# Optimization experiments

Hardware: AMD Instinct MI355X
Metric: run time of the kernel (lower is better)

The kernel has to match this reference:

```python
import jax, jax.numpy as jnp
import numpy as np
from jax import lax

N_NODES = 150_000
N_EDGES = 1_500_000
N_GRAPHS = 150          # batch_size(30) * sequence_length(5), hardcoded in forward
BATCH_SIZE = 30
SEQ_LEN = 5
IN_F = 1
HID = 100               # gcn_hidden_size == lstm_hidden_size


def setup_inputs() -> dict:
    key = jax.random.key(0)
    ks = jax.random.split(key, 12)
    x = jax.random.normal(ks[0], (N_NODES, IN_F), dtype=jnp.float32)
    edge_index = jax.random.randint(ks[1], (2, N_EDGES), 0, N_NODES, dtype=jnp.int32)
    # 150 graphs of 1000 nodes each (contiguous, as PyG batching produces)
    batch = jnp.repeat(jnp.arange(N_GRAPHS, dtype=jnp.int32), N_NODES // N_GRAPHS)
    s = 0.1
    params = {
        # GCNConv layer 1: Linear(no bias) weight stored [in, out]; separate bias
        "W1": jax.random.normal(ks[2], (IN_F, HID), jnp.float32) * s,
        "b1": jnp.zeros((HID,), jnp.float32),
        # GCNConv layer 2
        "W2": jax.random.normal(ks[3], (HID, HID), jnp.float32) * s,
        "b2": jnp.zeros((HID,), jnp.float32),
        # LSTM (PyTorch gate order i,f,g,o), weights [4H, in]/[4H, H]
        "W_ih": jax.random.normal(ks[4], (4 * HID, HID), jnp.float32) * s,
        "W_hh": jax.random.normal(ks[5], (4 * HID, HID), jnp.float32) * s,
        "b_ih": jnp.zeros((4 * HID,), jnp.float32),
        "b_hh": jnp.zeros((4 * HID,), jnp.float32),
        # output head Linear(HID, 1)
        "W_out": jax.random.normal(ks[6], (1, HID), jnp.float32) * s,
        "b_out": jnp.zeros((1,), jnp.float32),
    }
    return {"x": x, "edge_index": edge_index, "batch": batch, **params}


def _gcn_conv(x, src, dst, W, b, n_nodes):
    """PyG GCNConv: h = W x; out = D^-1/2 (A+I) D^-1/2 h + b."""
    h = x @ W  # [N, HID]
    deg = jax.ops.segment_sum(jnp.ones_like(dst, dtype=h.dtype), dst, num_segments=n_nodes)
    dinv = lax.rsqrt(deg)  # deg >= 1 thanks to self loops
    norm = dinv[src] * dinv[dst]  # [E+N]
    msg = h[src] * norm[:, None]  # gather + scale (memory-bound hot loop)
    out = jax.ops.segment_sum(msg, dst, num_segments=n_nodes)
    return out + b


def _lstm_last_hidden(xs, W_ih, W_hh, b_ih, b_hh):
    """xs: [B, T, H] -> last hidden state [B, H] (single-layer LSTM)."""
    B = xs.shape[0]
    H = W_hh.shape[1]
    h0 = jnp.zeros((B, H), xs.dtype)
    c0 = jnp.zeros((B, H), xs.dtype)

    def step(carry, xt):
        h, c = carry
        gates = xt @ W_ih.T + h @ W_hh.T + (b_ih + b_hh)
        i, f, g, o = jnp.split(gates, 4, axis=-1)
        c = jax.nn.sigmoid(f) * c + jax.nn.sigmoid(i) * jnp.tanh(g)
        h = jax.nn.sigmoid(o) * jnp.tanh(c)
        return (h, c), None

    (h_last, _), _ = lax.scan(step, (h0, c0), jnp.swapaxes(xs, 0, 1))
    return h_last


def reference(x, edge_index, batch, W1, b1, W2, b2, W_ih, W_hh, b_ih, b_hh, W_out, b_out):
    n_nodes = x.shape[0]
    loops = jnp.arange(n_nodes, dtype=edge_index.dtype)
    src = jnp.concatenate([edge_index[0], loops])
    dst = jnp.concatenate([edge_index[1], loops])

    h = _gcn_conv(x, src, dst, W1, b1, n_nodes)
    h = _gcn_conv(h, src, dst, W2, b2, n_nodes)

    # global mean pool over 150 graphs
    sums = jax.ops.segment_sum(h, batch, num_segments=N_GRAPHS)
    cnts = jax.ops.segment_sum(jnp.ones((n_nodes,), h.dtype), batch, num_segments=N_GRAPHS)
    pooled = sums / jnp.maximum(cnts, 1.0)[:, None]  # [150, HID]

    seq = pooled.reshape(BATCH_SIZE, SEQ_LEN, -1)  # [30, 5, HID]
    h_last = _lstm_last_hidden(seq, W_ih, W_hh, b_ih, b_hh)
    prediction = h_last @ W_out.T + b_out  # [30, 1]
    return prediction
```

## Files before the change

### kernel.cpp

```cpp
#include <hip/hip_runtime.h>
#include <math.h>

#define N_NODES   150000
#define N_EDGES   1500000
#define N_GRAPHS  150
#define HID       100
#define BATCH     30
#define SEQ       5
#define NODES_PER_GRAPH 1000

#define NPB       256
#define NB        ((N_NODES + NPB - 1) / NPB)
#define SBLK      512
#define EPB       2932

__global__ __launch_bounds__(256) void k_s1(const int* __restrict__ dst,
                                            int* __restrict__ blockBase) {
    __shared__ int hist[NB];
    int t = threadIdx.x;
    for (int i = t; i < NB; i += 256) hist[i] = 0;
    __syncthreads();
    int base = blockIdx.x * EPB;
    int end  = min(base + EPB, N_EDGES);
    for (int i = base + t * 4; i < end; i += 1024) {
        int4 d = *reinterpret_cast<const int4*>(dst + i);
        atomicAdd(&hist[d.x >> 8], 1);
        atomicAdd(&hist[d.y >> 8], 1);
        atomicAdd(&hist[d.z >> 8], 1);
        atomicAdd(&hist[d.w >> 8], 1);
    }
    __syncthreads();
    for (int j = t; j < NB; j += 256)
        blockBase[blockIdx.x * NB + j] = hist[j];
}

__global__ __launch_bounds__(512) void k_colscan(int* __restrict__ blockBase,
                                                 int* __restrict__ bucketCount) {
    __shared__ int v[SBLK];
    int j = blockIdx.x;
    int t = threadIdx.x;
    int val = blockBase[t * NB + j];
    v[t] = val;
    __syncthreads();
    for (int off = 1; off < SBLK; off <<= 1) {
        int w = (t >= off) ? v[t - off] : 0;
        __syncthreads();
        v[t] += w;
        __syncthreads();
    }
    blockBase[t * NB + j] = v[t] - val;
    if (t == SBLK - 1) bucketCount[j] = v[t];
}

__global__ __launch_bounds__(256) void k_scan(const int* __restrict__ cnt,
                                              int* __restrict__ start) {
    __shared__ int part[256];
    int t = threadIdx.x;
    int j0 = t * 3;
    int s = 0;
    #pragma unroll
    for (int k = 0; k < 3; ++k) { int j = j0 + k; if (j < NB) s += cnt[j]; }
    part[t] = s;
    __syncthreads();
    for (int off = 1; off < 256; off <<= 1) {
        int w = (t >= off) ? part[t - off] : 0;
        __syncthreads();
        part[t] += w;
        __syncthreads();
    }
    int run = part[t] - s;
    #pragma unroll
    for (int k = 0; k < 3; ++k) {
        int j = j0 + k;
        if (j < NB) { start[j] = run; run += cnt[j]; }
    }
    if (t == 0) start[NB] = N_EDGES;
}

__global__ __launch_bounds__(256) void k_s2(const int* __restrict__ src,
                                            const int* __restrict__ dst,
                                            const int* __restrict__ bucketStart,
                                            const int* __restrict__ blockBase,
                                            unsigned int* __restrict__ sorted) {
    __shared__ int cursor[NB];
    __shared__ int baseS[NB];
    int t = threadIdx.x;
    const int* bb = blockBase + blockIdx.x * NB;
    for (int i = t; i < NB; i += 256) {
        cursor[i] = 0;
        baseS[i] = bucketStart[i] + bb[i];
    }
    __syncthreads();
    int base = blockIdx.x * EPB;
    int end  = min(base + EPB, N_EDGES);
    for (int i = base + t * 4; i < end; i += 1024) {
        int4 s4 = *reinterpret_cast<const int4*>(src + i);
        int4 d4 = *reinterpret_cast<const int4*>(dst + i);
        int bs[4] = { d4.x >> 8, d4.y >> 8, d4.z >> 8, d4.w >> 8 };
        int sv[4] = { s4.x, s4.y, s4.z, s4.w };
        int dl[4] = { d4.x & 255, d4.y & 255, d4.z & 255, d4.w & 255 };
        #pragma unroll
        for (int k = 0; k < 4; ++k) {
            int b = bs[k];
            int idx = atomicAdd(&cursor[b], 1);
            sorted[baseS[b] + idx] = ((unsigned int)sv[k] << 8) | (unsigned int)dl[k];
        }
    }
}

__global__ __launch_bounds__(256) void k_accA(const unsigned int* __restrict__ sorted,
                                              const int* __restrict__ bucketStart,
                                              const float* __restrict__ x,
                                              float2* __restrict__ p) {
    __shared__ int degI[2][NPB];
    int b = blockIdx.x;
    int t = threadIdx.x;
    int n0 = b << 8;
    int nn = min(NPB, N_NODES - n0);
    degI[0][t] = 0; degI[1][t] = 0;
    __syncthreads();
    int e0 = bucketStart[b], e1 = bucketStart[b + 1];
    int rep = t & 1;
    int e0a = min((e0 + 3) & ~3, e1);
    if (e0 + t < e0a) atomicAdd(&degI[rep][sorted[e0 + t] & 255], 1);
    int nvec = (e1 - e0a) >> 2;
    for (int v = t; v < nvec; v += 256) {
        uint4 u4 = *reinterpret_cast<const uint4*>(sorted + e0a + v * 4);
        atomicAdd(&degI[rep][u4.x & 255], 1);
        atomicAdd(&degI[rep][u4.y & 255], 1);
        atomicAdd(&degI[rep][u4.z & 255], 1);
        atomicAdd(&degI[rep][u4.w & 255], 1);
    }
    int tail0 = e0a + (nvec << 2);
    if (tail0 + t < e1) atomicAdd(&degI[rep][sorted[tail0 + t] & 255], 1);
    __syncthreads();
    if (t < nn) {
        float dv = 1.0f / sqrtf((float)(1 + degI[0][t] + degI[1][t]));
        p[n0 + t] = make_float2(dv, dv * x[n0 + t]);
    }
}

__global__ __launch_bounds__(256) void k_accB(const unsigned int* __restrict__ sorted,
                                              const int* __restrict__ bucketStart,
                                              const float2* __restrict__ p,
                                              float* __restrict__ agg1,
                                              float* __restrict__ wsum,
                                              float* __restrict__ a1s) {
    __shared__ float t1[2][NPB], t2[2][NPB];
    int b = blockIdx.x;
    int t = threadIdx.x;
    int n0 = b << 8;
    int nn = min(NPB, N_NODES - n0);
    t1[0][t] = 0.0f; t1[1][t] = 0.0f; t2[0][t] = 0.0f; t2[1][t] = 0.0f;
    __syncthreads();
    int e0 = bucketStart[b], e1 = bucketStart[b + 1];
    int rep = t & 1;
    int e0a = min((e0 + 3) & ~3, e1);
    if (e0 + t < e0a) {
        unsigned int u = sorted[e0 + t];
        float2 pv = p[u >> 8];
        atomicAdd(&t2[rep][u & 255], pv.x);
        atomicAdd(&t1[rep][u & 255], pv.y);
    }
    int nvec = (e1 - e0a) >> 2;
    for (int v = t; v < nvec; v += 256) {
        uint4 u4 = *reinterpret_cast<const uint4*>(sorted + e0a + v * 4);
        float2 p0 = p[u4.x >> 8];
        float2 p1 = p[u4.y >> 8];
        float2 p2 = p[u4.z >> 8];
        float2 p3 = p[u4.w >> 8];
        atomicAdd(&t2[rep][u4.x & 255], p0.x);
        atomicAdd(&t1[rep][u4.x & 255], p0.y);
        atomicAdd(&t2[rep][u4.y & 255], p1.x);
        atomicAdd(&t1[rep][u4.y & 255], p1.y);
        atomicAdd(&t2[rep][u4.z & 255], p2.x);
        atomicAdd(&t1[rep][u4.z & 255], p2.y);
        atomicAdd(&t2[rep][u4.w & 255], p3.x);
        atomicAdd(&t1[rep][u4.w & 255], p3.y);
    }
    int tail0 = e0a + (nvec << 2);
    if (tail0 + t < e1) {
        unsigned int u = sorted[tail0 + t];
        float2 pv = p[u >> 8];
        atomicAdd(&t2[rep][u & 255], pv.x);
        atomicAdd(&t1[rep][u & 255], pv.y);
    }
    __syncthreads();
    if (t < nn) {
        float2 pv = p[n0 + t];
        float dv = pv.x;
        float T1 = t1[0][t] + t1[1][t];
        float T2 = t2[0][t] + t2[1][t];
        float a = dv * T1 + dv * pv.y;
        agg1[n0 + t] = a;
        wsum[n0 + t] = dv * (T2 + dv);
        a1s[n0 + t]  = dv * a;
    }
}

__global__ __launch_bounds__(256) void k_accC(const unsigned int* __restrict__ sorted,
                                              const int* __restrict__ bucketStart,
                                              const float2* __restrict__ p,
                                              const float* __restrict__ agg1,
                                              const float* __restrict__ a1s,
                                              float* __restrict__ agg2) {
    __shared__ float ua[2][NPB];
    int b = blockIdx.x;
    int t = threadIdx.x;
    int n0 = b << 8;
    int nn = min(NPB, N_NODES - n0);
    ua[0][t] = 0.0f; ua[1][t] = 0.0f;
    __syncthreads();
    int e0 = bucketStart[b], e1 = bucketStart[b + 1];
    int rep = t & 1;
    int e0a = min((e0 + 3) & ~3, e1);
    if (e0 + t < e0a) {
        unsigned int u = sorted[e0 + t];
        atomicAdd(&ua[rep][u & 255], a1s[u >> 8]);
    }
    int nvec = (e1 - e0a) >> 2;
    for (int v = t; v < nvec; v += 256) {
        uint4 u4 = *reinterpret_cast<const uint4*>(sorted + e0a + v * 4);
        atomicAdd(&ua[rep][u4.x & 255], a1s[u4.x >> 8]);
        atomicAdd(&ua[rep][u4.y & 255], a1s[u4.y >> 8]);
        atomicAdd(&ua[rep][u4.z & 255], a1s[u4.z >> 8]);
        atomicAdd(&ua[rep][u4.w & 255], a1s[u4.w >> 8]);
    }
    int tail0 = e0a + (nvec << 2);
    if (tail0 + t < e1) {
        unsigned int u = sorted[tail0 + t];
        atomicAdd(&ua[rep][u & 255], a1s[u >> 8]);
    }
    __syncthreads();
    if (t < nn) {
        float dv = p[n0 + t].x;
        agg2[n0 + t] = dv * (ua[0][t] + ua[1][t] + dv * agg1[n0 + t]);
    }
}

__global__ __launch_bounds__(512) void k_pre(const float* __restrict__ agg2,
                                             const float* __restrict__ wsum,
                                             const float* __restrict__ W1,
                                             const float* __restrict__ b1,
                                             const float* __restrict__ W2,
                                             const float* __restrict__ b2,
                                             const float* __restrict__ W_ih,
                                             const float* __restrict__ b_ih,
                                             const float* __restrict__ b_hh,
                                             float* __restrict__ Xg) {
    int g = blockIdx.x;
    int t = threadIdx.x;
    __shared__ float xs[HID];
    __shared__ float red_a[512], red_w[512];

    const float* pa = agg2 + (size_t)g * NODES_PER_GRAPH;
    const float* pw = wsum + (size_t)g * NODES_PER_GRAPH;
    float sa = 0.0f, sw = 0.0f;
    for (int n = t; n < NODES_PER_GRAPH; n += 512) { sa += pa[n]; sw += pw[n]; }
    red_a[t] = sa; red_w[t] = sw;
    __syncthreads();
    for (int s = 256; s > 0; s >>= 1) {
        if (t < s) { red_a[t] += red_a[t + s]; red_w[t] += red_w[t + s]; }
        __syncthreads();
    }
    float mean_a = red_a[0] * (1.0f / NODES_PER_GRAPH);
    float mean_w = red_w[0] * (1.0f / NODES_PER_GRAPH);

    if (t < HID) {
        float a = 0.0f, c = 0.0f;
        for (int k = 0; k < HID; ++k) {
            float w2 = W2[k * HID + t];
            a += W1[k] * w2;
            c += b1[k] * w2;
        }
        xs[t] = mean_a * a + mean_w * c + b2[t];
    }
    __syncthreads();

    if (t < 4 * HID) {
        float acc = b_ih[t] + b_hh[t];
        const float4* wp = reinterpret_cast<const float4*>(W_ih + t * HID);
        #pragma unroll
        for (int q = 0; q < HID / 4; ++q) {
            float4 w4 = wp[q];
            acc += xs[4*q+0] * w4.x + xs[4*q+1] * w4.y + xs[4*q+2] * w4.z + xs[4*q+3] * w4.w;
        }
        Xg[(size_t)g * 4 * HID + t] = acc;
    }
}

__global__ __launch_bounds__(512) void k_rec(const float* __restrict__ Xg,
                                             const float* __restrict__ W_hh,
                                             const float* __restrict__ W_out,
                                             const float* __restrict__ b_out,
                                             float* __restrict__ outp) {
    int b = blockIdx.x;
    int t = threadIdx.x;
    __shared__ float hs[HID], cs[HID];
    __shared__ float gsb[4 * HID];
    __shared__ float red[512];

    float wreg[HID];
    if (t < 4 * HID) {
        const float4* wp = reinterpret_cast<const float4*>(W_hh + t * HID);
        #pragma unroll
        for (int q = 0; q < HID / 4; ++q) {
            float4 w4 = wp[q];
            wreg[4*q+0] = w4.x; wreg[4*q+1] = w4.y; wreg[4*q+2] = w4.z; wreg[4*q+3] = w4.w;
        }
    }
    if (t < HID) { hs[t] = 0.0f; cs[t] = 0.0f; }
    __syncthreads();

    for (int step = 0; step < SEQ; ++step) {
        if (t < 4 * HID) {
            float acc = Xg[(size_t)(b * SEQ + step) * 4 * HID + t];
            #pragma unroll
            for (int k = 0; k < HID; ++k)
                acc += hs[k] * wreg[k];
            gsb[t] = acc;
        }
        __syncthreads();
        if (t < HID) {
            float ig = 1.0f / (1.0f + expf(-gsb[t]));
            float fg = 1.0f / (1.0f + expf(-gsb[HID + t]));
            float gg = tanhf(gsb[2 * HID + t]);
            float og = 1.0f / (1.0f + expf(-gsb[3 * HID + t]));
            float c  = fg * cs[t] + ig * gg;
            cs[t] = c;
            hs[t] = og * tanhf(c);
        }
        __syncthreads();
    }

    float v = (t < HID) ? hs[t] * W_out[t] : 0.0f;
    red[t] = v;
    __syncthreads();
    for (int s = 256; s > 0; s >>= 1) {
        if (t < s) red[t] += red[t + s];
        __syncthreads();
    }
    if (t == 0) outp[b] = red[0] + b_out[0];
}

static inline char* align_up(char* p, size_t a) {
    return (char*)(((uintptr_t)p + (a - 1)) & ~(uintptr_t)(a - 1));
}

extern "C" void kernel_launch(void* const* d_in, const int* in_sizes, int n_in,
                              void* d_out, int out_size, void* d_ws, size_t ws_size,
                              hipStream_t stream) {
    const float* x    = (const float*)d_in[0];
    const int*   ei   = (const int*)d_in[1];
    const int*   srcp = ei;
    const int*   dstp = ei + N_EDGES;
    const float* W1   = (const float*)d_in[3];
    const float* b1   = (const float*)d_in[4];
    const float* W2   = (const float*)d_in[5];
    const float* b2   = (const float*)d_in[6];
    const float* W_ih = (const float*)d_in[7];
    const float* W_hh = (const float*)d_in[8];
    const float* b_ih = (const float*)d_in[9];
    const float* b_hh = (const float*)d_in[10];
    const float* W_out= (const float*)d_in[11];
    const float* b_out= (const float*)d_in[12];
    float* out = (float*)d_out;

    char* w = (char*)d_ws;
    int*  bucketCount = (int*)w;            w = align_up(w + NB * sizeof(int), 64);
    int*  bucketStart = (int*)w;            w = align_up(w + (NB + 1) * sizeof(int), 64);
    int*  blockBase   = (int*)w;            w = align_up(w + (size_t)SBLK * NB * sizeof(int), 64);
    unsigned int* sorted = (unsigned int*)w; w = align_up(w + (size_t)N_EDGES * sizeof(unsigned int), 64);
    float2* p   = (float2*)w;               w = align_up(w + (size_t)N_NODES * sizeof(float2), 64);
    float* agg1 = (float*)w;                w = align_up(w + (size_t)N_NODES * sizeof(float), 64);
    float* wsum = (float*)w;                w = align_up(w + (size_t)N_NODES * sizeof(float), 64);
    float* a1s  = (float*)w;                w = align_up(w + (size_t)N_NODES * sizeof(float), 64);
    float* agg2 = (float*)w;                w = align_up(w + (size_t)N_NODES * sizeof(float), 64);
    float* Xg   = (float*)w;                w = align_up(w + (size_t)N_GRAPHS * 4 * HID * sizeof(float), 64);

    k_s1     <<<SBLK, 256, 0, stream>>>(dstp, blockBase);
    k_colscan<<<NB, SBLK, 0, stream>>>(blockBase, bucketCount);
    k_scan   <<<1, 256, 0, stream>>>(bucketCount, bucketStart);
    k_s2     <<<SBLK, 256, 0, stream>>>(srcp, dstp, bucketStart, blockBase, sorted);
    k_accA   <<<NB, 256, 0, stream>>>(sorted, bucketStart, x, p);
    k_accB   <<<NB, 256, 0, stream>>>(sorted, bucketStart, p, agg1, wsum, a1s);
    k_accC   <<<NB, 256, 0, stream>>>(sorted, bucketStart, p, agg1, a1s, agg2);
    k_pre    <<<N_GRAPHS, 512, 0, stream>>>(agg2, wsum, W1, b1, W2, b2, W_ih, b_ih, b_hh, Xg);
    k_rec    <<<BATCH, 512, 0, stream>>>(Xg, W_hh, W_out, b_out, out);
}
```

Before: 95.90 us.

## Fold mean-pool into per-graph atomic sums and fuse pre-LSTM into recurrence kernel

Rewrites the second aggregation so it never materializes per-node agg2 or wsum. Each block reduces its edge contributions straight into per-graph sums with atomics, using the fact that pooling is linear. The graph-level gate projection is merged into the LSTM kernel, removing one launch and the Xg round trip. The float2 gather of (dv, dv*x) becomes a single float gather in the first aggregation, at the cost of extra block reductions and global float atomics whose summation order is nondeterministic.

```diff
diff --git a/kernel.cpp b/kernel.cpp
--- a/kernel.cpp
+++ b/kernel.cpp
@@ -53,9 +53,12 @@
 }
 
 __global__ __launch_bounds__(256) void k_scan(const int* __restrict__ cnt,
-                                              int* __restrict__ start) {
+                                              int* __restrict__ start,
+                                              float* __restrict__ graphA,
+                                              float* __restrict__ graphW) {
     __shared__ int part[256];
     int t = threadIdx.x;
+    if (t < N_GRAPHS) { graphA[t] = 0.0f; graphW[t] = 0.0f; }
     int j0 = t * 3;
     int s = 0;
     #pragma unroll
@@ -108,11 +111,34 @@
     }
 }
 
+__device__ __forceinline__ void graph_reduce_add(float val, int thresh, int nn,
+                                                 int g0, float* red, int t,
+                                                 float* __restrict__ gdst) {
+    red[t] = (t < thresh) ? val : 0.0f;
+    __syncthreads();
+    for (int s = 128; s > 0; s >>= 1) {
+        if (t < s) red[t] += red[t + s];
+        __syncthreads();
+    }
+    if (t == 0) atomicAdd(&gdst[g0], red[0]);
+    __syncthreads();
+    red[t] = (t >= thresh) ? val : 0.0f;
+    __syncthreads();
+    for (int s = 128; s > 0; s >>= 1) {
+        if (t < s) red[t] += red[t + s];
+        __syncthreads();
+    }
+    if (t == 0 && thresh < nn) atomicAdd(&gdst[g0 + 1], red[0]);
+}
+
 __global__ __launch_bounds__(256) void k_accA(const unsigned int* __restrict__ sorted,
                                               const int* __restrict__ bucketStart,
                                               const float* __restrict__ x,
-                                              float2* __restrict__ p) {
+                                              float* __restrict__ pd,
+                                              float* __restrict__ px,
+                                              float* __restrict__ graphW) {
     __shared__ int degI[2][NPB];
+    __shared__ float red[256];
     int b = blockIdx.x;
     int t = threadIdx.x;
     int n0 = b << 8;
@@ -134,137 +160,144 @@
     int tail0 = e0a + (nvec << 2);
     if (tail0 + t < e1) atomicAdd(&degI[rep][sorted[tail0 + t] & 255], 1);
     __syncthreads();
+    float val = 0.0f;
     if (t < nn) {
         float dv = 1.0f / sqrtf((float)(1 + degI[0][t] + degI[1][t]));
-        p[n0 + t] = make_float2(dv, dv * x[n0 + t]);
-    }
+        pd[n0 + t] = dv;
+        px[n0 + t] = dv * x[n0 + t];
+        val = dv * dv;
+    }
+    int g0 = n0 / 1000;
+    int thresh = (g0 + 1) * 1000 - n0;
+    graph_reduce_add(val, thresh, nn, g0, red, t, graphW);
 }
 
 __global__ __launch_bounds__(256) void k_accB(const unsigned int* __restrict__ sorted,
                                               const int* __restrict__ bucketStart,
-                                              const float2* __restrict__ p,
-                                              float* __restrict__ agg1,
-                                              float* __restrict__ wsum,
-                                              float* __restrict__ a1s) {
-    __shared__ float t1[2][NPB], t2[2][NPB];
+                                              const float* __restrict__ pd,
+                                              const float* __restrict__ px,
+                                              float2* __restrict__ pa2,
+                                              float* __restrict__ graphA) {
+    __shared__ float t1[2][NPB];
+    __shared__ float red[256];
     int b = blockIdx.x;
     int t = threadIdx.x;
     int n0 = b << 8;
     int nn = min(NPB, N_NODES - n0);
-    t1[0][t] = 0.0f; t1[1][t] = 0.0f; t2[0][t] = 0.0f; t2[1][t] = 0.0f;
+    t1[0][t] = 0.0f; t1[1][t] = 0.0f;
     __syncthreads();
     int e0 = bucketStart[b], e1 = bucketStart[b + 1];
     int rep = t & 1;
     int e0a = min((e0 + 3) & ~3, e1);
     if (e0 + t < e0a) {
         unsigned int u = sorted[e0 + t];
-        float2 pv = p[u >> 8];
-        atomicAdd(&t2[rep][u & 255], pv.x);
-        atomicAdd(&t1[rep][u & 255], pv.y);
+        atomicAdd(&t1[rep][u & 255], px[u >> 8]);
     }
     int nvec = (e1 - e0a) >> 2;
     for (int v = t; v < nvec; v += 256) {
         uint4 u4 = *reinterpret_cast<const uint4*>(sorted + e0a + v * 4);
-        float2 p0 = p[u4.x >> 8];
-        float2 p1 = p[u4.y >> 8];
-        float2 p2 = p[u4.z >> 8];
-        float2 p3 = p[u4.w >> 8];
-        atomicAdd(&t2[rep][u4.x & 255], p0.x);
-        atomicAdd(&t1[rep][u4.x & 255], p0.y);
-        atomicAdd(&t2[rep][u4.y & 255], p1.x);
-        atomicAdd(&t1[rep][u4.y & 255], p1.y);
-        atomicAdd(&t2[rep][u4.z & 255], p2.x);
-        atomicAdd(&t1[rep][u4.z & 255], p2.y);
-        atomicAdd(&t2[rep][u4.w & 255], p3.x);
-        atomicAdd(&t1[rep][u4.w & 255], p3.y);
+        float p0 = px[u4.x >> 8];
+        float p1 = px[u4.y >> 8];
+        float p2 = px[u4.z >> 8];
+        float p3 = px[u4.w >> 8];
+        atomicAdd(&t1[rep][u4.x & 255], p0);
+        atomicAdd(&t1[rep][u4.y & 255], p1);
+        atomicAdd(&t1[rep][u4.z & 255], p2);
+        atomicAdd(&t1[rep][u4.w & 255], p3);
     }
     int tail0 = e0a + (nvec << 2);
     if (tail0 + t < e1) {
         unsigned int u = sorted[tail0 + t];
-        float2 pv = p[u >> 8];
-        atomicAdd(&t2[rep][u & 255], pv.x);
-        atomicAdd(&t1[rep][u & 255], pv.y);
-    }
-    __syncthreads();
+        atomicAdd(&t1[rep][u & 255], px[u >> 8]);
+    }
+    __syncthreads();
+    float val = 0.0f;
     if (t < nn) {
-        float2 pv = p[n0 + t];
-        float dv = pv.x;
+        float dv = pd[n0 + t];
         float T1 = t1[0][t] + t1[1][t];
-        float T2 = t2[0][t] + t2[1][t];
-        float a = dv * T1 + dv * pv.y;
-        agg1[n0 + t] = a;
-        wsum[n0 + t] = dv * (T2 + dv);
-        a1s[n0 + t]  = dv * a;
-    }
-}
-
-__global__ __launch_bounds__(256) void k_accC(const unsigned int* __restrict__ sorted,
+        float agg1 = dv * T1 + dv * px[n0 + t];
+        float a1 = dv * agg1;
+        pa2[n0 + t] = make_float2(dv, a1);
+        val = dv * a1;
+    }
+    int g0 = n0 / 1000;
+    int thresh = (g0 + 1) * 1000 - n0;
+    graph_reduce_add(val, thresh, nn, g0, red, t, graphA);
+}
+
+__global__ __launch_bounds__(256) void k_accG(const unsigned int* __restrict__ sorted,
                                               const int* __restrict__ bucketStart,
-                                              const float2* __restrict__ p,
-                                              const float* __restrict__ agg1,
-                                              const float* __restrict__ a1s,
-                                              float* __restrict__ agg2) {
-    __shared__ float ua[2][NPB];
+                                              const float* __restrict__ pd,
+                                              const float2* __restrict__ pa2,
+                                              float* __restrict__ graphA,
+                                              float* __restrict__ graphW) {
+    __shared__ float dvl[NPB];
+    __shared__ float4 red4[256];
     int b = blockIdx.x;
     int t = threadIdx.x;
     int n0 = b << 8;
     int nn = min(NPB, N_NODES - n0);
-    ua[0][t] = 0.0f; ua[1][t] = 0.0f;
-    __syncthreads();
+    dvl[t] = (t < nn) ? pd[n0 + t] : 0.0f;
+    __syncthreads();
+    int g0 = n0 / 1000;
+    int thresh = (g0 + 1) * 1000 - n0;
+    float sa0 = 0.f, sa1 = 0.f, sw0 = 0.f, sw1 = 0.f;
     int e0 = bucketStart[b], e1 = bucketStart[b + 1];
-    int rep = t & 1;
     int e0a = min((e0 + 3) & ~3, e1);
-    if (e0 + t < e0a) {
-        unsigned int u = sorted[e0 + t];
-        atomicAdd(&ua[rep][u & 255], a1s[u >> 8]);
-    }
+    auto proc = [&](unsigned int u) {
+        int dl = (int)(u & 255);
+        float dvd = dvl[dl];
+        float2 v = pa2[u >> 8];
+        if (dl < thresh) { sw0 += dvd * v.x; sa0 += dvd * v.y; }
+        else             { sw1 += dvd * v.x; sa1 += dvd * v.y; }
+    };
+    if (e0 + t < e0a) proc(sorted[e0 + t]);
     int nvec = (e1 - e0a) >> 2;
     for (int v = t; v < nvec; v += 256) {
         uint4 u4 = *reinterpret_cast<const uint4*>(sorted + e0a + v * 4);
-        atomicAdd(&ua[rep][u4.x & 255], a1s[u4.x >> 8]);
-        atomicAdd(&ua[rep][u4.y & 255], a1s[u4.y >> 8]);
-        atomicAdd(&ua[rep][u4.z & 255], a1s[u4.z >> 8]);
-        atomicAdd(&ua[rep][u4.w & 255], a1s[u4.w >> 8]);
+        proc(u4.x); proc(u4.y); proc(u4.z); proc(u4.w);
     }
     int tail0 = e0a + (nvec << 2);
-    if (tail0 + t < e1) {
-        unsigned int u = sorted[tail0 + t];
-        atomicAdd(&ua[rep][u & 255], a1s[u >> 8]);
-    }
-    __syncthreads();
-    if (t < nn) {
-        float dv = p[n0 + t].x;
-        agg2[n0 + t] = dv * (ua[0][t] + ua[1][t] + dv * agg1[n0 + t]);
-    }
-}
-
-__global__ __launch_bounds__(512) void k_pre(const float* __restrict__ agg2,
-                                             const float* __restrict__ wsum,
-                                             const float* __restrict__ W1,
-                                             const float* __restrict__ b1,
-                                             const float* __restrict__ W2,
-                                             const float* __restrict__ b2,
-                                             const float* __restrict__ W_ih,
-                                             const float* __restrict__ b_ih,
-                                             const float* __restrict__ b_hh,
-                                             float* __restrict__ Xg) {
-    int g = blockIdx.x;
-    int t = threadIdx.x;
-    __shared__ float xs[HID];
-    __shared__ float red_a[512], red_w[512];
-
-    const float* pa = agg2 + (size_t)g * NODES_PER_GRAPH;
-    const float* pw = wsum + (size_t)g * NODES_PER_GRAPH;
-    float sa = 0.0f, sw = 0.0f;
-    for (int n = t; n < NODES_PER_GRAPH; n += 512) { sa += pa[n]; sw += pw[n]; }
-    red_a[t] = sa; red_w[t] = sw;
-    __syncthreads();
-    for (int s = 256; s > 0; s >>= 1) {
-        if (t < s) { red_a[t] += red_a[t + s]; red_w[t] += red_w[t + s]; }
-        __syncthreads();
-    }
-    float mean_a = red_a[0] * (1.0f / NODES_PER_GRAPH);
-    float mean_w = red_w[0] * (1.0f / NODES_PER_GRAPH);
+    if (tail0 + t < e1) proc(sorted[tail0 + t]);
+    red4[t] = make_float4(sa0, sa1, sw0, sw1);
+    __syncthreads();
+    for (int s = 128; s > 0; s >>= 1) {
+        if (t < s) {
+            red4[t].x += red4[t + s].x; red4[t].y += red4[t + s].y;
+            red4[t].z += red4[t + s].z; red4[t].w += red4[t + s].w;
+        }
+        __syncthreads();
+    }
+    if (t == 0) {
+        atomicAdd(&graphA[g0], red4[0].x);
+        atomicAdd(&graphW[g0], red4[0].z);
+        if (thresh < nn) {
+            atomicAdd(&graphA[g0 + 1], red4[0].y);
+            atomicAdd(&graphW[g0 + 1], red4[0].w);
+        }
+    }
+}
+
+__global__ __launch_bounds__(512) void k_tail(const float* __restrict__ graphA,
+                                              const float* __restrict__ graphW,
+                                              const float* __restrict__ W1,
+                                              const float* __restrict__ b1,
+                                              const float* __restrict__ W2,
+                                              const float* __restrict__ b2,
+                                              const float* __restrict__ W_ih,
+                                              const float* __restrict__ W_hh,
+                                              const float* __restrict__ b_ih,
+                                              const float* __restrict__ b_hh,
+                                              const float* __restrict__ W_out,
+                                              const float* __restrict__ b_out,
+                                              float* __restrict__ outp) {
+    int b = blockIdx.x;
+    int t = threadIdx.x;
+    __shared__ float v1[HID], v2[HID];
+    __shared__ float xs_l[SEQ][HID];
+    __shared__ float Xg_l[SEQ][4 * HID];
+    __shared__ float hs[HID], cs[HID], gsb[4 * HID];
+    __shared__ float red[512];
 
     if (t < HID) {
         float a = 0.0f, c = 0.0f;
@@ -273,36 +306,36 @@
             a += W1[k] * w2;
             c += b1[k] * w2;
         }
-        xs[t] = mean_a * a + mean_w * c + b2[t];
-    }
-    __syncthreads();
-
+        v1[t] = a; v2[t] = c;
+    }
+    __syncthreads();
+
+    if (t < SEQ * HID) {
+        int s = t / HID, j = t - s * HID;
+        int g = b * SEQ + s;
+        float ma = graphA[g] * (1.0f / NODES_PER_GRAPH);
+        float mw = graphW[g] * (1.0f / NODES_PER_GRAPH);
+        xs_l[s][j] = ma * v1[j] + mw * v2[j] + b2[j];
+    }
+    __syncthreads();
+
+    float wreg[HID];
     if (t < 4 * HID) {
-        float acc = b_ih[t] + b_hh[t];
         const float4* wp = reinterpret_cast<const float4*>(W_ih + t * HID);
         #pragma unroll
         for (int q = 0; q < HID / 4; ++q) {
             float4 w4 = wp[q];
-            acc += xs[4*q+0] * w4.x + xs[4*q+1] * w4.y + xs[4*q+2] * w4.z + xs[4*q+3] * w4.w;
-        }
-        Xg[(size_t)g * 4 * HID + t] = acc;
-    }
-}
-
-__global__ __launch_bounds__(512) void k_rec(const float* __restrict__ Xg,
-                                             const float* __restrict__ W_hh,
-                                             const float* __restrict__ W_out,
-                                             const float* __restrict__ b_out,
-                                             float* __restrict__ outp) {
-    int b = blockIdx.x;
-    int t = threadIdx.x;
-    __shared__ float hs[HID], cs[HID];
-    __shared__ float gsb[4 * HID];
-    __shared__ float red[512];
-
-    float wreg[HID];
-    if (t < 4 * HID) {
-        const float4* wp = reinterpret_cast<const float4*>(W_hh + t * HID);
+            wreg[4*q+0] = w4.x; wreg[4*q+1] = w4.y; wreg[4*q+2] = w4.z; wreg[4*q+3] = w4.w;
+        }
+        float bias = b_ih[t] + b_hh[t];
+        for (int s = 0; s < SEQ; ++s) {
+            float acc = bias;
+            #pragma unroll
+            for (int k = 0; k < HID; ++k)
+                acc += xs_l[s][k] * wreg[k];
+            Xg_l[s][t] = acc;
+        }
+        wp = reinterpret_cast<const float4*>(W_hh + t * HID);
         #pragma unroll
         for (int q = 0; q < HID / 4; ++q) {
             float4 w4 = wp[q];
@@ -314,7 +347,7 @@
 
     for (int step = 0; step < SEQ; ++step) {
         if (t < 4 * HID) {
-            float acc = Xg[(size_t)(b * SEQ + step) * 4 * HID + t];
+            float acc = Xg_l[step][t];
             #pragma unroll
             for (int k = 0; k < HID; ++k)
                 acc += hs[k] * wreg[k];
@@ -367,24 +400,23 @@
     float* out = (float*)d_out;
 
     char* w = (char*)d_ws;
-    int*  bucketCount = (int*)w;            w = align_up(w + NB * sizeof(int), 64);
-    int*  bucketStart = (int*)w;            w = align_up(w + (NB + 1) * sizeof(int), 64);
-    int*  blockBase   = (int*)w;            w = align_up(w + (size_t)SBLK * NB * sizeof(int), 64);
+    int*  bucketCount = (int*)w;             w = align_up(w + NB * sizeof(int), 64);
+    int*  bucketStart = (int*)w;             w = align_up(w + (NB + 1) * sizeof(int), 64);
+    int*  blockBase   = (int*)w;             w = align_up(w + (size_t)SBLK * NB * sizeof(int), 64);
     unsigned int* sorted = (unsigned int*)w; w = align_up(w + (size_t)N_EDGES * sizeof(unsigned int), 64);
-    float2* p   = (float2*)w;               w = align_up(w + (size_t)N_NODES * sizeof(float2), 64);
-    float* agg1 = (float*)w;                w = align_up(w + (size_t)N_NODES * sizeof(float), 64);
-    float* wsum = (float*)w;                w = align_up(w + (size_t)N_NODES * sizeof(float), 64);
-    float* a1s  = (float*)w;                w = align_up(w + (size_t)N_NODES * sizeof(float), 64);
-    float* agg2 = (float*)w;                w = align_up(w + (size_t)N_NODES * sizeof(float), 64);
-    float* Xg   = (float*)w;                w = align_up(w + (size_t)N_GRAPHS * 4 * HID * sizeof(float), 64);
+    float*  pd   = (float*)w;                w = align_up(w + (size_t)N_NODES * sizeof(float), 64);
+    float*  px   = (float*)w;                w = align_up(w + (size_t)N_NODES * sizeof(float), 64);
+    float2* pa2  = (float2*)w;               w = align_up(w + (size_t)N_NODES * sizeof(float2), 64);
+    float* graphA = (float*)w;               w = align_up(w + N_GRAPHS * sizeof(float), 64);
+    float* graphW = (float*)w;               w = align_up(w + N_GRAPHS * sizeof(float), 64);
 
     k_s1     <<<SBLK, 256, 0, stream>>>(dstp, blockBase);
     k_colscan<<<NB, SBLK, 0, stream>>>(blockBase, bucketCount);
-    k_scan   <<<1, 256, 0, stream>>>(bucketCount, bucketStart);
+    k_scan   <<<1, 256, 0, stream>>>(bucketCount, bucketStart, graphA, graphW);
     k_s2     <<<SBLK, 256, 0, stream>>>(srcp, dstp, bucketStart, blockBase, sorted);
-    k_accA   <<<NB, 256, 0, stream>>>(sorted, bucketStart, x, p);
-    k_accB   <<<NB, 256, 0, stream>>>(sorted, bucketStart, p, agg1, wsum, a1s);
-    k_accC   <<<NB, 256, 0, stream>>>(sorted, bucketStart, p, agg1, a1s, agg2);
-    k_pre    <<<N_GRAPHS, 512, 0, stream>>>(agg2, wsum, W1, b1, W2, b2, W_ih, b_ih, b_hh, Xg);
-    k_rec    <<<BATCH, 512, 0, stream>>>(Xg, W_hh, W_out, b_out, out);
-}
+    k_accA   <<<NB, 256, 0, stream>>>(sorted, bucketStart, x, pd, px, graphW);
+    k_accB   <<<NB, 256, 0, stream>>>(sorted, bucketStart, pd, px, pa2, graphA);
+    k_accG   <<<NB, 256, 0, stream>>>(sorted, bucketStart, pd, pa2, graphA, graphW);
+    k_tail   <<<BATCH, 512, 0, stream>>>(graphA, graphW, W1, b1, W2, b2,
+                                         W_ih, W_hh, b_ih, b_hh, W_out, b_out, out);
+}
```

Result: faster. 86.39 us (-9.9%).
